# Kernel optimization log

Measured on AMD Instinct MI355X. Metric: run time of the kernel, lower is better.

Reference implementation:

```python
import jax, jax.numpy as jnp
import numpy as np

H = 64      # num query heads
HKV = 8     # num key/value heads
D = 64      # head_dim
HID = 2880  # hidden_size
B = 8       # batch (num sequences)
Q = 16      # query tokens per sequence
P = 128     # kv pages per sequence
PAGE = 16   # kv page size
NPAGES = 2048  # total pages in cache pool
NEG = -1e9  # finite stand-in for -inf mask (avoids inf arithmetic; exp underflows to 0 identically)


def setup_inputs() -> dict:
    key = jax.random.key(0)
    ks = jax.random.split(key, 6)
    n = B * Q
    S = P * PAGE
    hidden_states = jax.random.normal(ks[0], (n, HID), jnp.float32) * 0.02
    kv_cache_at_layer = jax.random.normal(ks[1], (NPAGES, 2, PAGE, HKV, D), jnp.float32)
    qkv_dim = D * (H + 2 * HKV)
    w_qkv = jax.random.normal(ks[2], (qkv_dim, HID), jnp.float32) * 0.02
    b_qkv = jnp.zeros((qkv_dim,), jnp.float32)
    w_o = jax.random.normal(ks[3], (HID, H * D), jnp.float32) * 0.02
    b_o = jnp.zeros((HID,), jnp.float32)
    sinks = jax.random.normal(ks[4], (H,), jnp.float32)
    qo_indptr = (jnp.arange(B + 1) * Q).astype(jnp.int32)
    kv_page_indptr = (jnp.arange(B + 1) * P).astype(jnp.int32)
    kv_last_page_lens = jnp.full((B,), PAGE, jnp.int32)
    kv_page_indices = jnp.asarray(np.random.default_rng(0).permutation(NPAGES)[:B * P], jnp.int32)
    # causal mask: query i of each sequence sits at absolute position S - Q + i
    qpos = S - Q + jnp.arange(Q)
    mask = jnp.where(jnp.arange(S)[None, :] <= qpos[:, None], 0.0, NEG).astype(jnp.float32)
    attention_mask = jnp.broadcast_to(mask[None], (B, Q, S)).reshape(-1)
    return dict(hidden_states=hidden_states, kv_cache_at_layer=kv_cache_at_layer,
                attention_mask=attention_mask, w_qkv=w_qkv, b_qkv=b_qkv, w_o=w_o, b_o=b_o,
                sinks=sinks, qo_indptr=qo_indptr, kv_page_indptr=kv_page_indptr,
                kv_last_page_lens=kv_last_page_lens, kv_page_indices=kv_page_indices)


def reference(hidden_states, kv_cache_at_layer, attention_mask, w_qkv, b_qkv, w_o, b_o,
              sinks, qo_indptr, kv_page_indptr, kv_last_page_lens, kv_page_indices):
    n = hidden_states.shape[0]
    b = qo_indptr.shape[0] - 1
    q_len = n // b                              # uniform ragged layout (see setup)
    p = kv_page_indices.shape[0] // b
    page = kv_cache_at_layer.shape[2]
    s = p * page
    g = H // HKV                                # query heads per kv head (GQA groups)
    scaling = D ** -0.5

    qkv = hidden_states @ w_qkv.T + b_qkv                       # [n, (H+2*HKV)*D]
    q = qkv[:, :H * D].reshape(b, q_len, HKV, g, D) * scaling    # [b q hkv g d]

    pages = kv_page_indices.reshape(b, p)
    k = kv_cache_at_layer[pages, 0].reshape(b, s, HKV, D)        # gather pages -> [b s hkv d]
    v = kv_cache_at_layer[pages, 1].reshape(b, s, HKV, D)

    scores = jnp.einsum('bqhgd,bshd->bhgqs', q, k).astype(jnp.float32)
    mask = attention_mask.reshape(b, q_len, s)
    # keys beyond the valid portion of the last page are invalid
    valid = jnp.arange(s)[None, :] < ((p - 1) * page + kv_last_page_lens[:, None])
    mask = jnp.where(valid[:, None, :], mask, NEG)
    scores = scores + mask[:, None, None, :, :]

    # online-softmax merge across pages is equivalent to this single pass;
    # running max starts at 0 in the original, hence the clamp to 0
    m = jnp.maximum(scores.max(axis=-1), 0.0)                    # [b hkv g q]
    pexp = jnp.exp(scores - m[..., None])                        # [b hkv g q s]
    sink = sinks.reshape(HKV, g).astype(jnp.float32)
    sum_exp = pexp.sum(axis=-1) + jnp.exp(sink[None, :, :, None] - m)
    num = jnp.einsum('bhgqs,bshd->bhgqd', pexp, v.astype(jnp.float32))
    attn = num / sum_exp[..., None]                              # [b hkv g q d]
    attn = attn.transpose(0, 3, 1, 2, 4).reshape(n, H * D)       # q (h d)
    return attn.astype(hidden_states.dtype) @ w_o.T + b_o
```

## Files before the change

kernel.cpp:

```cpp
#include <hip/hip_runtime.h>
#include <hip/hip_bf16.h>

#define BB      8
#define QL      16
#define NHKV    8
#define NG      8
#define DD      64
#define HIDN    2880
#define PP      128
#define PGSZ    16
#define SS      2048
#define NQ      4096
#define NSPLIT  8
#define KSQ     5
#define KCQ     576
#define KSO     8
#define KCO     512

typedef short bf16x8 __attribute__((ext_vector_type(8)));
typedef short short4v __attribute__((ext_vector_type(4)));
typedef float f32x4  __attribute__((ext_vector_type(4)));

__device__ inline short f2bf(float f) {
  __hip_bfloat16 h = __float2bfloat16(f);
  union { __hip_bfloat16 h; short s; } u; u.h = h;
  return u.s;
}

__device__ inline float bf2f(short s) {
  union { float f; unsigned u; } u;
  u.u = ((unsigned)(unsigned short)s) << 16;
  return u.f;
}

__device__ inline bf16x8 cvt8(float4 a, float4 b) {
  bf16x8 r;
  r[0] = f2bf(a.x); r[1] = f2bf(a.y); r[2] = f2bf(a.z); r[3] = f2bf(a.w);
  r[4] = f2bf(b.x); r[5] = f2bf(b.y); r[6] = f2bf(b.z); r[7] = f2bf(b.w);
  return r;
}

__device__ inline bf16x8 pack8(const float* __restrict__ p) {
  float4 a = *(const float4*)p;
  float4 b = *(const float4*)(p + 4);
  return cvt8(a, b);
}

__global__ __launch_bounds__(256) void k_qkv_split(const float* __restrict__ hid,
                                                   const float* __restrict__ wq,
                                                   short* __restrict__ qpart) {
  const int n0 = blockIdx.x * 32;
  const int ks = blockIdx.y;
  const int tid = threadIdx.x;
  const int wid = tid >> 6, lane = tid & 63;
  const int lo = lane & 15, hi = lane >> 4;
  const int m0 = wid * 32;

  const float* xr0 = hid + (size_t)(m0 + lo) * HIDN;
  const float* xr1 = hid + (size_t)(m0 + 16 + lo) * HIDN;
  const float* wr0 = wq + (size_t)(n0 + lo) * HIDN;
  const float* wr1 = wq + (size_t)(n0 + 16 + lo) * HIDN;
  const int kb = ks * KCQ + hi * 8;

  f32x4 acc[2][2];
#pragma unroll
  for (int mt = 0; mt < 2; ++mt)
#pragma unroll
    for (int nt = 0; nt < 2; ++nt) acc[mt][nt] = (f32x4){0.f, 0.f, 0.f, 0.f};

  float4 bufA[4][2], bufB[4][2];
#define LOADQ(dst, kk) { \
    dst[0][0] = *(const float4*)(xr0 + (kk));     dst[0][1] = *(const float4*)(xr0 + (kk) + 4); \
    dst[1][0] = *(const float4*)(xr1 + (kk));     dst[1][1] = *(const float4*)(xr1 + (kk) + 4); \
    dst[2][0] = *(const float4*)(wr0 + (kk));     dst[2][1] = *(const float4*)(wr0 + (kk) + 4); \
    dst[3][0] = *(const float4*)(wr1 + (kk));     dst[3][1] = *(const float4*)(wr1 + (kk) + 4); }
#define MFMAQ(buf) { \
    bf16x8 a0 = cvt8(buf[0][0], buf[0][1]); \
    bf16x8 a1 = cvt8(buf[1][0], buf[1][1]); \
    bf16x8 w0 = cvt8(buf[2][0], buf[2][1]); \
    bf16x8 w1 = cvt8(buf[3][0], buf[3][1]); \
    acc[0][0] = __builtin_amdgcn_mfma_f32_16x16x32_bf16(a0, w0, acc[0][0], 0, 0, 0); \
    acc[0][1] = __builtin_amdgcn_mfma_f32_16x16x32_bf16(a0, w1, acc[0][1], 0, 0, 0); \
    acc[1][0] = __builtin_amdgcn_mfma_f32_16x16x32_bf16(a1, w0, acc[1][0], 0, 0, 0); \
    acc[1][1] = __builtin_amdgcn_mfma_f32_16x16x32_bf16(a1, w1, acc[1][1], 0, 0, 0); }

  LOADQ(bufA, kb);
#pragma unroll
  for (int it = 0; it < 9; ++it) {
    const int kk = kb + it * 64;
    LOADQ(bufB, kk + 32);
    MFMAQ(bufA);
    if (it < 8) LOADQ(bufA, kk + 64);
    MFMAQ(bufB);
  }
#undef LOADQ
#undef MFMAQ

  short* qp = qpart + (size_t)ks * 128 * NQ;
#pragma unroll
  for (int mt = 0; mt < 2; ++mt)
#pragma unroll
    for (int nt = 0; nt < 2; ++nt)
#pragma unroll
      for (int r = 0; r < 4; ++r) {
        int m = m0 + mt * 16 + hi * 4 + r;
        int n = n0 + nt * 16 + lo;
        qp[(size_t)m * NQ + n] = f2bf(acc[mt][nt][r]);
      }
}

__global__ __launch_bounds__(256) void k_attn(const float* __restrict__ kvc,
                                              const int* __restrict__ pidx,
                                              const int* __restrict__ llen,
                                              const short* __restrict__ qpart,
                                              const float* __restrict__ bq,
                                              short* __restrict__ opart,
                                              float* __restrict__ lbuf) {
  const int blk = blockIdx.x;
  const int pair = blk >> 3, split = blk & 7;
  const int b = pair >> 3, kvh = pair & 7;
  const int tid = threadIdx.x;
  const int wid = tid >> 6, lane = tid & 63;
  const int lo = lane & 15, hi = lane >> 4;
  const int wrow = wid * 32;

  __shared__ short plds[128][72];
  __shared__ float vlds[64][65];

  bf16x8 qf[2][2];
#pragma unroll
  for (int mt = 0; mt < 2; ++mt) {
    int r = wrow + mt * 16 + lo;
    int g = r >> 4, qq = r & 15;
    int m = b * QL + qq;
    int h = kvh * NG + g;
#pragma unroll
    for (int kg = 0; kg < 2; ++kg) {
      int n = h * DD + kg * 32 + hi * 8;
      float4 b0 = *(const float4*)(bq + n);
      float4 b1 = *(const float4*)(bq + n + 4);
      float s[8];
      s[0] = b0.x; s[1] = b0.y; s[2] = b0.z; s[3] = b0.w;
      s[4] = b1.x; s[5] = b1.y; s[6] = b1.z; s[7] = b1.w;
#pragma unroll
      for (int k2 = 0; k2 < KSQ; ++k2) {
        bf16x8 p = *(const bf16x8*)(qpart + ((size_t)k2 * 128 + m) * NQ + n);
#pragma unroll
        for (int j = 0; j < 8; ++j) s[j] += bf2f(p[j]);
      }
      bf16x8 q8;
#pragma unroll
      for (int j = 0; j < 8; ++j) q8[j] = f2bf(s[j] * 0.125f);
      qf[mt][kg] = q8;
    }
  }

  float l_part[2][4];
  f32x4 o_acc[2][4];
#pragma unroll
  for (int mt = 0; mt < 2; ++mt)
#pragma unroll
    for (int j = 0; j < 4; ++j) l_part[mt][j] = 0.f;
#pragma unroll
  for (int mt = 0; mt < 2; ++mt)
#pragma unroll
    for (int dt = 0; dt < 4; ++dt) o_acc[mt][dt] = (f32x4){0.f, 0.f, 0.f, 0.f};

  const int sKeepEnd = (PP - 1) * PGSZ + llen[b];
  const int* pib = pidx + b * PP;
  const int sBeg = split * (SS / NSPLIT);
  const int sEnd = sBeg + (SS / NSPLIT);

  for (int s0 = sBeg; s0 < sEnd; s0 += 64) {
    float4 vreg[4];
    const int vsr = tid >> 4;
    const int vc4 = (tid & 15) * 4;
#pragma unroll
    for (int pc = 0; pc < 4; ++pc) {
      int pg = pib[(s0 >> 4) + pc];
      vreg[pc] = *(const float4*)(kvc +
          ((((size_t)pg * 2 + 1) * PGSZ + vsr) * NHKV + kvh) * DD + vc4);
    }

    f32x4 sc[2][4];
#pragma unroll
    for (int mt = 0; mt < 2; ++mt)
#pragma unroll
      for (int nt = 0; nt < 4; ++nt) sc[mt][nt] = (f32x4){0.f, 0.f, 0.f, 0.f};

#pragma unroll
    for (int nt = 0; nt < 4; ++nt) {
      int s = s0 + nt * 16 + lo;
      int pg = pib[s >> 4];
      const float* kp = kvc + ((((size_t)pg * 2 + 0) * PGSZ + (s & 15)) * NHKV + kvh) * DD;
#pragma unroll
      for (int kg = 0; kg < 2; ++kg) {
        bf16x8 kf = pack8(kp + kg * 32 + hi * 8);
        sc[0][nt] = __builtin_amdgcn_mfma_f32_16x16x32_bf16(qf[0][kg], kf, sc[0][nt], 0, 0, 0);
        sc[1][nt] = __builtin_amdgcn_mfma_f32_16x16x32_bf16(qf[1][kg], kf, sc[1][nt], 0, 0, 0);
      }
    }

    if (s0 + 64 > SS - QL) {
#pragma unroll
      for (int mt = 0; mt < 2; ++mt)
#pragma unroll
        for (int j = 0; j < 4; ++j) {
          int r = wrow + mt * 16 + hi * 4 + j;
          int qq = r & 15;
          int sLimQ = (SS - QL) + qq;
#pragma unroll
          for (int nt = 0; nt < 4; ++nt) {
            int s = s0 + nt * 16 + lo;
            bool keep = (s <= sLimQ) && (s < sKeepEnd);
            sc[mt][nt][j] = keep ? sc[mt][nt][j] : -1.0e9f;
          }
        }
    }

#pragma unroll
    for (int mt = 0; mt < 2; ++mt)
#pragma unroll
      for (int j = 0; j < 4; ++j)
#pragma unroll
        for (int nt = 0; nt < 4; ++nt) {
          float p = __expf(sc[mt][nt][j]);
          sc[mt][nt][j] = p;
          l_part[mt][j] += p;
        }

    __syncthreads();
#pragma unroll
    for (int pc = 0; pc < 4; ++pc) {
      int sl = pc * 16 + vsr;
      vlds[sl][vc4]     = vreg[pc].x;
      vlds[sl][vc4 + 1] = vreg[pc].y;
      vlds[sl][vc4 + 2] = vreg[pc].z;
      vlds[sl][vc4 + 3] = vreg[pc].w;
    }
#pragma unroll
    for (int mt = 0; mt < 2; ++mt)
#pragma unroll
      for (int j = 0; j < 4; ++j) {
        int r = wrow + mt * 16 + hi * 4 + j;
#pragma unroll
        for (int nt = 0; nt < 4; ++nt)
          plds[r][nt * 16 + lo] = f2bf(sc[mt][nt][j]);
      }
    __syncthreads();

#pragma unroll
    for (int kg = 0; kg < 2; ++kg) {
      bf16x8 pa[2];
      pa[0] = *(const bf16x8*)(&plds[wrow + lo][kg * 32 + hi * 8]);
      pa[1] = *(const bf16x8*)(&plds[wrow + 16 + lo][kg * 32 + hi * 8]);
#pragma unroll
      for (int dt = 0; dt < 4; ++dt) {
        bf16x8 vf;
#pragma unroll
        for (int j = 0; j < 8; ++j)
          vf[j] = f2bf(vlds[kg * 32 + hi * 8 + j][dt * 16 + lo]);
        o_acc[0][dt] = __builtin_amdgcn_mfma_f32_16x16x32_bf16(pa[0], vf, o_acc[0][dt], 0, 0, 0);
        o_acc[1][dt] = __builtin_amdgcn_mfma_f32_16x16x32_bf16(pa[1], vf, o_acc[1][dt], 0, 0, 0);
      }
    }
  }

#pragma unroll
  for (int mt = 0; mt < 2; ++mt)
#pragma unroll
    for (int j = 0; j < 4; ++j)
#pragma unroll
      for (int off = 1; off < 16; off <<= 1)
        l_part[mt][j] += __shfl_xor(l_part[mt][j], off, 64);

  short* op = opart + (size_t)(pair * NSPLIT + split) * 128 * DD;
#pragma unroll
  for (int mt = 0; mt < 2; ++mt)
#pragma unroll
    for (int dt = 0; dt < 4; ++dt)
#pragma unroll
      for (int j = 0; j < 4; ++j) {
        int r = wrow + mt * 16 + hi * 4 + j;
        op[r * DD + dt * 16 + lo] = f2bf(o_acc[mt][dt][j]);
      }
  if (lo == 0) {
#pragma unroll
    for (int mt = 0; mt < 2; ++mt)
#pragma unroll
      for (int j = 0; j < 4; ++j) {
        int r = wrow + mt * 16 + hi * 4 + j;
        lbuf[(size_t)(pair * NSPLIT + split) * 128 + r] = l_part[mt][j];
      }
  }
}

__global__ __launch_bounds__(256) void k_merge(const short* __restrict__ opart,
                                               const float* __restrict__ lbuf,
                                               const float* __restrict__ sinks,
                                               short* __restrict__ attnbf) {
  const int pair = blockIdx.x;
  const int b = pair >> 3, kvh = pair & 7;
  const int tid = threadIdx.x;

  __shared__ float Ls[128];
  if (tid < 128) {
    int r = tid, g = r >> 4;
    float L = __expf(sinks[kvh * NG + g]);
#pragma unroll
    for (int s2 = 0; s2 < NSPLIT; ++s2)
      L += lbuf[(size_t)(pair * NSPLIT + s2) * 128 + r];
    Ls[r] = L;
  }
  __syncthreads();

  for (int u = tid; u < 128 * 16; u += 256) {
    int r = u >> 4, c4 = (u & 15) * 4;
    float o0 = 0.f, o1 = 0.f, o2 = 0.f, o3 = 0.f;
#pragma unroll
    for (int s2 = 0; s2 < NSPLIT; ++s2) {
      short4v pv = *(const short4v*)(opart +
          ((size_t)(pair * NSPLIT + s2) * 128 + r) * DD + c4);
      o0 += bf2f(pv[0]); o1 += bf2f(pv[1]); o2 += bf2f(pv[2]); o3 += bf2f(pv[3]);
    }
    float inv = 1.0f / Ls[r];
    int g = r >> 4, qq = r & 15;
    int h = kvh * NG + g;
    short4v ov;
    ov[0] = f2bf(o0 * inv); ov[1] = f2bf(o1 * inv);
    ov[2] = f2bf(o2 * inv); ov[3] = f2bf(o3 * inv);
    *(short4v*)(attnbf + (size_t)(b * QL + qq) * NQ + h * DD + c4) = ov;
  }
}

__global__ __launch_bounds__(256) void k_out_split(const short* __restrict__ attnbf,
                                                   const float* __restrict__ wo,
                                                   short* __restrict__ outpart) {
  const int n0 = blockIdx.x * 32;
  const int ks = blockIdx.y;
  const int tid = threadIdx.x;
  const int wid = tid >> 6, lane = tid & 63;
  const int lo = lane & 15, hi = lane >> 4;
  const int m0 = wid * 32;

  const short* ar0 = attnbf + (size_t)(m0 + lo) * NQ;
  const short* ar1 = attnbf + (size_t)(m0 + 16 + lo) * NQ;
  const float* wr0 = wo + (size_t)(n0 + lo) * NQ;
  const float* wr1 = wo + (size_t)(n0 + 16 + lo) * NQ;
  const int kb = ks * KCO + hi * 8;

  f32x4 acc[2][2];
#pragma unroll
  for (int mt = 0; mt < 2; ++mt)
#pragma unroll
    for (int nt = 0; nt < 2; ++nt) acc[mt][nt] = (f32x4){0.f, 0.f, 0.f, 0.f};

  bf16x8 aA[2], aB[2];
  float4 wA[2][2], wB[2][2];
#define LOADO(adst, wdst, kk) { \
    adst[0] = *(const bf16x8*)(ar0 + (kk)); \
    adst[1] = *(const bf16x8*)(ar1 + (kk)); \
    wdst[0][0] = *(const float4*)(wr0 + (kk)); wdst[0][1] = *(const float4*)(wr0 + (kk) + 4); \
    wdst[1][0] = *(const float4*)(wr1 + (kk)); wdst[1][1] = *(const float4*)(wr1 + (kk) + 4); }
#define MFMAO(abuf, wbuf) { \
    bf16x8 w0 = cvt8(wbuf[0][0], wbuf[0][1]); \
    bf16x8 w1 = cvt8(wbuf[1][0], wbuf[1][1]); \
    acc[0][0] = __builtin_amdgcn_mfma_f32_16x16x32_bf16(abuf[0], w0, acc[0][0], 0, 0, 0); \
    acc[0][1] = __builtin_amdgcn_mfma_f32_16x16x32_bf16(abuf[0], w1, acc[0][1], 0, 0, 0); \
    acc[1][0] = __builtin_amdgcn_mfma_f32_16x16x32_bf16(abuf[1], w0, acc[1][0], 0, 0, 0); \
    acc[1][1] = __builtin_amdgcn_mfma_f32_16x16x32_bf16(abuf[1], w1, acc[1][1], 0, 0, 0); }

  LOADO(aA, wA, kb);
#pragma unroll
  for (int it = 0; it < 8; ++it) {
    const int kk = kb + it * 64;
    LOADO(aB, wB, kk + 32);
    MFMAO(aA, wA);
    if (it < 7) LOADO(aA, wA, kk + 64);
    MFMAO(aB, wB);
  }
#undef LOADO
#undef MFMAO

  short* op = outpart + (size_t)ks * 128 * HIDN;
#pragma unroll
  for (int mt = 0; mt < 2; ++mt)
#pragma unroll
    for (int nt = 0; nt < 2; ++nt)
#pragma unroll
      for (int r = 0; r < 4; ++r) {
        int m = m0 + mt * 16 + hi * 4 + r;
        int n = n0 + nt * 16 + lo;
        op[(size_t)m * HIDN + n] = f2bf(acc[mt][nt][r]);
      }
}

__global__ __launch_bounds__(256) void k_ored(const short* __restrict__ outpart,
                                              const float* __restrict__ bo,
                                              float* __restrict__ out) {
  int idx = blockIdx.x * 256 + threadIdx.x;
  int m = idx / 720;
  int n = (idx - m * 720) * 4;
  float4 v = *(const float4*)(bo + n);
#pragma unroll
  for (int ks = 0; ks < KSO; ++ks) {
    short4v p = *(const short4v*)(outpart + ((size_t)ks * 128 + m) * HIDN + n);
    v.x += bf2f(p[0]); v.y += bf2f(p[1]); v.z += bf2f(p[2]); v.w += bf2f(p[3]);
  }
  *(float4*)(out + (size_t)m * HIDN + n) = v;
}

extern "C" void kernel_launch(void* const* d_in, const int* in_sizes, int n_in,
                              void* d_out, int out_size, void* d_ws, size_t ws_size,
                              hipStream_t stream) {
  const float* hid   = (const float*)d_in[0];
  const float* kvc   = (const float*)d_in[1];
  const float* wq    = (const float*)d_in[3];
  const float* bq    = (const float*)d_in[4];
  const float* wo    = (const float*)d_in[5];
  const float* bo    = (const float*)d_in[6];
  const float* sinks = (const float*)d_in[7];
  const int* llen    = (const int*)d_in[10];
  const int* pidx    = (const int*)d_in[11];
  float* out = (float*)d_out;

  char* ws = (char*)d_ws;
  short* qpart   = (short*)(ws + 0);
  short* attnbf  = (short*)(ws + 5242880);
  short* opart   = (short*)(ws + 6291456);
  float* lbuf    = (float*)(ws + 14680064);
  short* outpart = (short*)(ws + 14942208);

  k_qkv_split<<<dim3(128, KSQ), dim3(256), 0, stream>>>(hid, wq, qpart);
  k_attn<<<dim3(BB * NHKV * NSPLIT), dim3(256), 0, stream>>>(kvc, pidx, llen, qpart, bq, opart, lbuf);
  k_merge<<<dim3(BB * NHKV), dim3(256), 0, stream>>>(opart, lbuf, sinks, attnbf);
  k_out_split<<<dim3(HIDN / 32, KSO), dim3(256), 0, stream>>>(attnbf, wo, outpart);
  k_ored<<<dim3(360), dim3(256), 0, stream>>>(outpart, bo, out);
}
```

Before: 127.9 us.

## Fuse split merge into attention via last-block counter and store V transposed bf16

Removes the separate merge kernel. Each attention block now bumps a per-pair atomic counter, and the last split to finish does the sink-weighted merge of the partial outputs in place. V is converted to bf16 and written transposed into shared memory, so the PV MFMA operand becomes one vector LDS load instead of eight scalar loads plus conversions. It also adds a memset launch to reset the counters, plus fence and atomic overhead, and the merge work now runs serially on only one block per pair.

```diff
diff --git a/kernel.cpp b/kernel.cpp
--- a/kernel.cpp
+++ b/kernel.cpp
@@ -70,10 +70,10 @@
 
   float4 bufA[4][2], bufB[4][2];
 #define LOADQ(dst, kk) { \
-    dst[0][0] = *(const float4*)(xr0 + (kk));     dst[0][1] = *(const float4*)(xr0 + (kk) + 4); \
-    dst[1][0] = *(const float4*)(xr1 + (kk));     dst[1][1] = *(const float4*)(xr1 + (kk) + 4); \
-    dst[2][0] = *(const float4*)(wr0 + (kk));     dst[2][1] = *(const float4*)(wr0 + (kk) + 4); \
-    dst[3][0] = *(const float4*)(wr1 + (kk));     dst[3][1] = *(const float4*)(wr1 + (kk) + 4); }
+    dst[0][0] = *(const float4*)(xr0 + (kk)); dst[0][1] = *(const float4*)(xr0 + (kk) + 4); \
+    dst[1][0] = *(const float4*)(xr1 + (kk)); dst[1][1] = *(const float4*)(xr1 + (kk) + 4); \
+    dst[2][0] = *(const float4*)(wr0 + (kk)); dst[2][1] = *(const float4*)(wr0 + (kk) + 4); \
+    dst[3][0] = *(const float4*)(wr1 + (kk)); dst[3][1] = *(const float4*)(wr1 + (kk) + 4); }
 #define MFMAQ(buf) { \
     bf16x8 a0 = cvt8(buf[0][0], buf[0][1]); \
     bf16x8 a1 = cvt8(buf[1][0], buf[1][1]); \
@@ -114,8 +114,11 @@
                                               const int* __restrict__ llen,
                                               const short* __restrict__ qpart,
                                               const float* __restrict__ bq,
+                                              const float* __restrict__ sinks,
                                               short* __restrict__ opart,
-                                              float* __restrict__ lbuf) {
+                                              float* __restrict__ lbuf,
+                                              short* __restrict__ attnbf,
+                                              unsigned* __restrict__ cnt) {
   const int blk = blockIdx.x;
   const int pair = blk >> 3, split = blk & 7;
   const int b = pair >> 3, kvh = pair & 7;
@@ -124,8 +127,10 @@
   const int lo = lane & 15, hi = lane >> 4;
   const int wrow = wid * 32;
 
-  __shared__ short plds[128][72];
-  __shared__ float vlds[64][65];
+  __shared__ short plds[128][68];
+  __shared__ short vtlds[64][68];
+  __shared__ float Ls[128];
+  __shared__ int lastFlag;
 
   bf16x8 qf[2][2];
 #pragma unroll
@@ -137,11 +142,11 @@
 #pragma unroll
     for (int kg = 0; kg < 2; ++kg) {
       int n = h * DD + kg * 32 + hi * 8;
-      float4 b0 = *(const float4*)(bq + n);
-      float4 b1 = *(const float4*)(bq + n + 4);
+      float4 bb0 = *(const float4*)(bq + n);
+      float4 bb1 = *(const float4*)(bq + n + 4);
       float s[8];
-      s[0] = b0.x; s[1] = b0.y; s[2] = b0.z; s[3] = b0.w;
-      s[4] = b1.x; s[5] = b1.y; s[6] = b1.z; s[7] = b1.w;
+      s[0] = bb0.x; s[1] = bb0.y; s[2] = bb0.z; s[3] = bb0.w;
+      s[4] = bb1.x; s[5] = bb1.y; s[6] = bb1.z; s[7] = bb1.w;
 #pragma unroll
       for (int k2 = 0; k2 < KSQ; ++k2) {
         bf16x8 p = *(const bf16x8*)(qpart + ((size_t)k2 * 128 + m) * NQ + n);
@@ -172,12 +177,14 @@
   const int sEnd = sBeg + (SS / NSPLIT);
 
   for (int s0 = sBeg; s0 < sEnd; s0 += 64) {
+    const int p0 = s0 >> 4;
+
     float4 vreg[4];
     const int vsr = tid >> 4;
     const int vc4 = (tid & 15) * 4;
 #pragma unroll
     for (int pc = 0; pc < 4; ++pc) {
-      int pg = pib[(s0 >> 4) + pc];
+      int pg = pib[p0 + pc];
       vreg[pc] = *(const float4*)(kvc +
           ((((size_t)pg * 2 + 1) * PGSZ + vsr) * NHKV + kvh) * DD + vc4);
     }
@@ -190,9 +197,8 @@
 
 #pragma unroll
     for (int nt = 0; nt < 4; ++nt) {
-      int s = s0 + nt * 16 + lo;
-      int pg = pib[s >> 4];
-      const float* kp = kvc + ((((size_t)pg * 2 + 0) * PGSZ + (s & 15)) * NHKV + kvh) * DD;
+      int pg = pib[p0 + nt];
+      const float* kp = kvc + ((((size_t)pg * 2 + 0) * PGSZ + lo) * NHKV + kvh) * DD;
 #pragma unroll
       for (int kg = 0; kg < 2; ++kg) {
         bf16x8 kf = pack8(kp + kg * 32 + hi * 8);
@@ -233,10 +239,10 @@
 #pragma unroll
     for (int pc = 0; pc < 4; ++pc) {
       int sl = pc * 16 + vsr;
-      vlds[sl][vc4]     = vreg[pc].x;
-      vlds[sl][vc4 + 1] = vreg[pc].y;
-      vlds[sl][vc4 + 2] = vreg[pc].z;
-      vlds[sl][vc4 + 3] = vreg[pc].w;
+      vtlds[vc4    ][sl] = f2bf(vreg[pc].x);
+      vtlds[vc4 + 1][sl] = f2bf(vreg[pc].y);
+      vtlds[vc4 + 2][sl] = f2bf(vreg[pc].z);
+      vtlds[vc4 + 3][sl] = f2bf(vreg[pc].w);
     }
 #pragma unroll
     for (int mt = 0; mt < 2; ++mt)
@@ -256,10 +262,7 @@
       pa[1] = *(const bf16x8*)(&plds[wrow + 16 + lo][kg * 32 + hi * 8]);
 #pragma unroll
       for (int dt = 0; dt < 4; ++dt) {
-        bf16x8 vf;
-#pragma unroll
-        for (int j = 0; j < 8; ++j)
-          vf[j] = f2bf(vlds[kg * 32 + hi * 8 + j][dt * 16 + lo]);
+        bf16x8 vf = *(const bf16x8*)(&vtlds[dt * 16 + lo][kg * 32 + hi * 8]);
         o_acc[0][dt] = __builtin_amdgcn_mfma_f32_16x16x32_bf16(pa[0], vf, o_acc[0][dt], 0, 0, 0);
         o_acc[1][dt] = __builtin_amdgcn_mfma_f32_16x16x32_bf16(pa[1], vf, o_acc[1][dt], 0, 0, 0);
       }
@@ -293,17 +296,18 @@
         lbuf[(size_t)(pair * NSPLIT + split) * 128 + r] = l_part[mt][j];
       }
   }
-}
-
-__global__ __launch_bounds__(256) void k_merge(const short* __restrict__ opart,
-                                               const float* __restrict__ lbuf,
-                                               const float* __restrict__ sinks,
-                                               short* __restrict__ attnbf) {
-  const int pair = blockIdx.x;
-  const int b = pair >> 3, kvh = pair & 7;
-  const int tid = threadIdx.x;
-
-  __shared__ float Ls[128];
+
+  __threadfence();
+  __syncthreads();
+  if (tid == 0) {
+    unsigned old = __hip_atomic_fetch_add(&cnt[pair], 1u, __ATOMIC_ACQ_REL,
+                                          __HIP_MEMORY_SCOPE_AGENT);
+    lastFlag = (old == NSPLIT - 1);
+  }
+  __syncthreads();
+  if (!lastFlag) return;
+  __threadfence();
+
   if (tid < 128) {
     int r = tid, g = r >> 4;
     float L = __expf(sinks[kvh * NG + g]);
@@ -363,12 +367,12 @@
     wdst[0][0] = *(const float4*)(wr0 + (kk)); wdst[0][1] = *(const float4*)(wr0 + (kk) + 4); \
     wdst[1][0] = *(const float4*)(wr1 + (kk)); wdst[1][1] = *(const float4*)(wr1 + (kk) + 4); }
 #define MFMAO(abuf, wbuf) { \
-    bf16x8 w0 = cvt8(wbuf[0][0], wbuf[0][1]); \
-    bf16x8 w1 = cvt8(wbuf[1][0], wbuf[1][1]); \
-    acc[0][0] = __builtin_amdgcn_mfma_f32_16x16x32_bf16(abuf[0], w0, acc[0][0], 0, 0, 0); \
-    acc[0][1] = __builtin_amdgcn_mfma_f32_16x16x32_bf16(abuf[0], w1, acc[0][1], 0, 0, 0); \
-    acc[1][0] = __builtin_amdgcn_mfma_f32_16x16x32_bf16(abuf[1], w0, acc[1][0], 0, 0, 0); \
-    acc[1][1] = __builtin_amdgcn_mfma_f32_16x16x32_bf16(abuf[1], w1, acc[1][1], 0, 0, 0); }
+    bf16x8 ww0 = cvt8(wbuf[0][0], wbuf[0][1]); \
+    bf16x8 ww1 = cvt8(wbuf[1][0], wbuf[1][1]); \
+    acc[0][0] = __builtin_amdgcn_mfma_f32_16x16x32_bf16(abuf[0], ww0, acc[0][0], 0, 0, 0); \
+    acc[0][1] = __builtin_amdgcn_mfma_f32_16x16x32_bf16(abuf[0], ww1, acc[0][1], 0, 0, 0); \
+    acc[1][0] = __builtin_amdgcn_mfma_f32_16x16x32_bf16(abuf[1], ww0, acc[1][0], 0, 0, 0); \
+    acc[1][1] = __builtin_amdgcn_mfma_f32_16x16x32_bf16(abuf[1], ww1, acc[1][1], 0, 0, 0); }
 
   LOADO(aA, wA, kb);
 #pragma unroll
@@ -425,15 +429,17 @@
   float* out = (float*)d_out;
 
   char* ws = (char*)d_ws;
-  short* qpart   = (short*)(ws + 0);
-  short* attnbf  = (short*)(ws + 5242880);
-  short* opart   = (short*)(ws + 6291456);
-  float* lbuf    = (float*)(ws + 14680064);
-  short* outpart = (short*)(ws + 14942208);
-
+  short*    qpart   = (short*)(ws + 0);
+  short*    attnbf  = (short*)(ws + 5242880);
+  short*    opart   = (short*)(ws + 6291456);
+  float*    lbuf    = (float*)(ws + 14680064);
+  short*    outpart = (short*)(ws + 14942208);
+  unsigned* cnt     = (unsigned*)(ws + 20840448);
+
+  hipMemsetAsync(cnt, 0, 256, stream);
   k_qkv_split<<<dim3(128, KSQ), dim3(256), 0, stream>>>(hid, wq, qpart);
-  k_attn<<<dim3(BB * NHKV * NSPLIT), dim3(256), 0, stream>>>(kvc, pidx, llen, qpart, bq, opart, lbuf);
-  k_merge<<<dim3(BB * NHKV), dim3(256), 0, stream>>>(opart, lbuf, sinks, attnbf);
+  k_attn<<<dim3(BB * NHKV * NSPLIT), dim3(256), 0, stream>>>(
+      kvc, pidx, llen, qpart, bq, sinks, opart, lbuf, attnbf, cnt);
   k_out_split<<<dim3(HIDN / 32, KSO), dim3(256), 0, stream>>>(attnbf, wo, outpart);
   k_ored<<<dim3(360), dim3(256), 0, stream>>>(outpart, bo, out);
 }
```

New measurement: 223.3 us. 74.6% more time.
